# Kernel optimization log

Measured on AMD Instinct MI355X. Metric: run time of the kernel, lower is better.

## Reference

```python
import jax, jax.numpy as jnp
import numpy as np

B, N, F_IN, F_OUT, K, E = 4, 50000, 64, 64, 4, 800000


def setup_inputs() -> dict:
    key = jax.random.key(0)
    ks = jax.random.split(key, 6)
    x = jax.random.normal(ks[0], (B, N, F_IN), dtype=jnp.float32)
    support_rows = jax.random.randint(ks[1], (K, E), 0, N, dtype=jnp.int32)
    support_cols = jax.random.randint(ks[2], (K, E), 0, N, dtype=jnp.int32)
    support_vals = jax.random.normal(ks[3], (K, E), dtype=jnp.float32) * 0.1
    kernels = jax.random.normal(ks[4], (K, F_IN, F_OUT), dtype=jnp.float32) * (1.0 / np.sqrt(F_IN))
    bias = jnp.zeros((F_OUT,), dtype=jnp.float32)
    return {"x": x, "support_rows": support_rows, "support_cols": support_cols,
            "support_vals": support_vals, "kernels": kernels, "bias": bias}


def reference(x, support_rows, support_cols, support_vals, kernels, bias):
    # dropout_rate = 0.0 -> identity; sum_k support_k @ (x @ W_k) + bias, relu
    n = x.shape[1]
    out = jnp.zeros(x.shape[:2] + (kernels.shape[-1],), dtype=x.dtype)
    for k in range(kernels.shape[0]):  # small fixed K = 4 Chebyshev supports
        h = jnp.einsum('bnf,fg->bng', x, kernels[k])          # dense projection
        msg = h[:, support_cols[k], :] * support_vals[k][None, :, None]  # [B,E,G]
        agg = jax.ops.segment_sum(jnp.swapaxes(msg, 0, 1), support_rows[k],
                                  num_segments=n)              # [N,B,G]
        out = out + jnp.swapaxes(agg, 0, 1)
    return jax.nn.relu(out + bias)
```

## Files before the change

### kernel.cpp

```cpp
#include <hip/hip_runtime.h>


#define FDIM 64

__device__ __forceinline__ unsigned short bf16_rne(float v) {
    unsigned u = __float_as_uint(v);
    return (unsigned short)((u + 0x7FFFu + ((u >> 16) & 1u)) >> 16);
}

__global__ __launch_bounds__(256) void gemm_all(
    const float* __restrict__ x, const float* __restrict__ kernels,
    unsigned short* __restrict__ hb, int M, int kbase, int kcount)
{
    __shared__ float xs[64][68];
    __shared__ float Wl[64][64];

    const int t = threadIdx.x;
    const int row0 = blockIdx.x * 64;

#pragma unroll
    for (int i = 0; i < 4; ++i) {
        int idx = t + 256 * i;
        int r = idx >> 4;
        int c4 = idx & 15;
        float4 v = ((const float4*)(x + (size_t)(row0 + r) * FDIM))[c4];
        int f = c4 * 4;
        xs[f + 0][r] = v.x;
        xs[f + 1][r] = v.y;
        xs[f + 2][r] = v.z;
        xs[f + 3][r] = v.w;
    }

    const int r0 = (t >> 4) * 4;
    const int g0 = (t & 15) * 4;

    for (int kk = 0; kk < kcount; ++kk) {
        __syncthreads();
        {
            const float4* Wv = (const float4*)(kernels + (size_t)(kbase + kk) * FDIM * FDIM);
            float4* Wd = (float4*)&Wl[0][0];
#pragma unroll
            for (int i = 0; i < 4; ++i) Wd[t + 256 * i] = Wv[t + 256 * i];
        }
        __syncthreads();

        float acc[4][4];
#pragma unroll
        for (int i = 0; i < 4; ++i)
#pragma unroll
            for (int j = 0; j < 4; ++j) acc[i][j] = 0.f;

#pragma unroll
        for (int f = 0; f < 64; ++f) {
            float4 xv = *(const float4*)&xs[f][r0];
            float4 wv = *(const float4*)&Wl[f][g0];
            acc[0][0] = fmaf(xv.x, wv.x, acc[0][0]);
            acc[0][1] = fmaf(xv.x, wv.y, acc[0][1]);
            acc[0][2] = fmaf(xv.x, wv.z, acc[0][2]);
            acc[0][3] = fmaf(xv.x, wv.w, acc[0][3]);
            acc[1][0] = fmaf(xv.y, wv.x, acc[1][0]);
            acc[1][1] = fmaf(xv.y, wv.y, acc[1][1]);
            acc[1][2] = fmaf(xv.y, wv.z, acc[1][2]);
            acc[1][3] = fmaf(xv.y, wv.w, acc[1][3]);
            acc[2][0] = fmaf(xv.z, wv.x, acc[2][0]);
            acc[2][1] = fmaf(xv.z, wv.y, acc[2][1]);
            acc[2][2] = fmaf(xv.z, wv.z, acc[2][2]);
            acc[2][3] = fmaf(xv.z, wv.w, acc[2][3]);
            acc[3][0] = fmaf(xv.w, wv.x, acc[3][0]);
            acc[3][1] = fmaf(xv.w, wv.y, acc[3][1]);
            acc[3][2] = fmaf(xv.w, wv.z, acc[3][2]);
            acc[3][3] = fmaf(xv.w, wv.w, acc[3][3]);
        }

#pragma unroll
        for (int i = 0; i < 4; ++i) {
            ushort4 p;
            p.x = bf16_rne(acc[i][0]);
            p.y = bf16_rne(acc[i][1]);
            p.z = bf16_rne(acc[i][2]);
            p.w = bf16_rne(acc[i][3]);
            *(ushort4*)(hb + ((size_t)kk * M + row0 + r0 + i) * FDIM + g0) = p;
        }
    }
}

__global__ __launch_bounds__(256) void hist_rows(
    const int* __restrict__ rows, int* __restrict__ counts,
    int total, int E, int N)
{
    int i = blockIdx.x * 256 + threadIdx.x;
    if (i >= total) return;
    int k = i / E;
    atomicAdd(&counts[k * N + rows[i]], 1);
}

__global__ __launch_bounds__(256) void scan_block_sums(
    const int* __restrict__ counts, int* __restrict__ bsums, int N, int nb)
{
    int k = blockIdx.x / nb, j = blockIdx.x % nb;
    int t = threadIdx.x, lane = t & 63, w = t >> 6;
    int i = j * 256 + t;
    int v = (i < N) ? counts[k * N + i] : 0;
#pragma unroll
    for (int off = 32; off; off >>= 1) v += __shfl_down(v, off);
    __shared__ int lds[4];
    if (lane == 0) lds[w] = v;
    __syncthreads();
    if (t == 0) bsums[k * nb + j] = lds[0] + lds[1] + lds[2] + lds[3];
}

__global__ __launch_bounds__(256) void scan_bsums(int* bsums, int nb, int K)
{
    __shared__ int lds[4];
    __shared__ int carry;
    int t = threadIdx.x, lane = t & 63, w = t >> 6;
    for (int k = 0; k < K; ++k) {
        if (t == 0) carry = 0;
        __syncthreads();
        for (int base = 0; base < nb; base += 256) {
            int i = base + t;
            int v = (i < nb) ? bsums[k * nb + i] : 0;
            int x = v;
#pragma unroll
            for (int off = 1; off < 64; off <<= 1) {
                int y = __shfl_up(x, off);
                if (lane >= off) x += y;
            }
            if (lane == 63) lds[w] = x;
            __syncthreads();
            int wo = 0;
            for (int q = 0; q < w; ++q) wo += lds[q];
            int excl = carry + wo + x - v;
            if (i < nb) bsums[k * nb + i] = excl;
            __syncthreads();
            if (t == 255) carry = carry + wo + x;
            __syncthreads();
        }
    }
}

__global__ __launch_bounds__(256) void scan_write_ptr(
    const int* __restrict__ counts, const int* __restrict__ bsums,
    int* __restrict__ row_ptr, int N, int nb)
{
    int k = blockIdx.x / nb, j = blockIdx.x % nb;
    int t = threadIdx.x, lane = t & 63, w = t >> 6;
    int i = j * 256 + t;
    int v = (i < N) ? counts[k * N + i] : 0;
    int x = v;
#pragma unroll
    for (int off = 1; off < 64; off <<= 1) {
        int y = __shfl_up(x, off);
        if (lane >= off) x += y;
    }
    __shared__ int lds[4];
    if (lane == 63) lds[w] = x;
    __syncthreads();
    int wo = 0;
    for (int q = 0; q < w; ++q) wo += lds[q];
    int incl = wo + x;
    if (i < N) row_ptr[k * (N + 1) + i + 1] = bsums[k * nb + j] + incl;
    if (t == 0 && j == 0) row_ptr[k * (N + 1)] = 0;
}

__global__ __launch_bounds__(256) void fill_csr_packed(
    const int* __restrict__ rows, const int* __restrict__ cols,
    const float* __restrict__ vals, const int* __restrict__ row_ptr,
    int* __restrict__ counts, unsigned* __restrict__ csr,
    int total, int E, int N)
{
    int i = blockIdx.x * 256 + threadIdx.x;
    if (i >= total) return;
    int k = i / E;
    int row = rows[i];
    int old = atomicSub(&counts[k * N + row], 1);
    int slot = row_ptr[k * (N + 1) + row] + old - 1;
    unsigned pk = ((unsigned)cols[i] << 16) | (unsigned)bf16_rne(vals[i]);
    csr[(size_t)k * E + slot] = pk;
}

__global__ __launch_bounds__(256) void gather_fused(
    const unsigned short* __restrict__ hb, const int* __restrict__ row_ptr,
    const unsigned* __restrict__ csr, const float* __restrict__ bias,
    float* __restrict__ out, int N, int M, int E,
    int kbase, int kcount, int first, int last)
{
    const int wid = (blockIdx.x << 2) | (threadIdx.x >> 6);
    if (wid >= N) return;
    const int lane = threadIdx.x & 63;
    const int b = lane >> 4;
    const int c4 = lane & 15;

    float4 acc = make_float4(0.f, 0.f, 0.f, 0.f);

    for (int kk = 0; kk < kcount; ++kk) {
        const int* rp = row_ptr + (size_t)(kbase + kk) * (N + 1);
        const unsigned* ck = csr + (size_t)(kbase + kk) * E;
        const unsigned short* hbb =
            hb + ((size_t)kk * M + (size_t)b * N) * FDIM + c4 * 4;

        const int e0 = rp[wid];
        const int e1 = rp[wid + 1];

        for (int base = e0; base < e1; base += 64) {
            const int n = min(64, e1 - base);
            unsigned w = 0;
            if (lane < n) w = ck[base + lane];
            for (int j = 0; j < n; ++j) {
                unsigned ww = __shfl((int)w, j);
                int col = ww >> 16;
                float val = __uint_as_float(ww << 16);
                uint2 hv = *(const uint2*)(hbb + (size_t)col * FDIM);
                float f0 = __uint_as_float(hv.x << 16);
                float f1 = __uint_as_float(hv.x & 0xFFFF0000u);
                float f2 = __uint_as_float(hv.y << 16);
                float f3 = __uint_as_float(hv.y & 0xFFFF0000u);
                acc.x = fmaf(f0, val, acc.x);
                acc.y = fmaf(f1, val, acc.y);
                acc.z = fmaf(f2, val, acc.z);
                acc.w = fmaf(f3, val, acc.w);
            }
        }
    }

    float* op = out + ((size_t)b * N + wid) * FDIM + c4 * 4;
    if (first && last) {
        float4 bi = ((const float4*)bias)[c4];
        float4 o;
        o.x = fmaxf(acc.x + bi.x, 0.f);
        o.y = fmaxf(acc.y + bi.y, 0.f);
        o.z = fmaxf(acc.z + bi.z, 0.f);
        o.w = fmaxf(acc.w + bi.w, 0.f);
        *(float4*)op = o;
    } else if (first) {
        *(float4*)op = acc;
    } else if (!last) {
        float4 o = *(const float4*)op;
        o.x += acc.x; o.y += acc.y; o.z += acc.z; o.w += acc.w;
        *(float4*)op = o;
    } else {
        float4 o = *(const float4*)op;
        float4 bi = ((const float4*)bias)[c4];
        o.x = fmaxf(o.x + acc.x + bi.x, 0.f);
        o.y = fmaxf(o.y + acc.y + bi.y, 0.f);
        o.z = fmaxf(o.z + acc.z + bi.z, 0.f);
        o.w = fmaxf(o.w + acc.w + bi.w, 0.f);
        *(float4*)op = o;
    }
}

__global__ __launch_bounds__(256) void gemm64(
    const float* __restrict__ x, const float* __restrict__ W,
    float* __restrict__ h, int M)
{
    __shared__ float xs[64][68];
    __shared__ float Wl[64][64];
    const int t = threadIdx.x;
    {
        const float4* Wv = (const float4*)W;
        float4* Wd = (float4*)&Wl[0][0];
#pragma unroll
        for (int i = 0; i < 4; ++i) Wd[t + 256 * i] = Wv[t + 256 * i];
    }
    const int row0 = blockIdx.x * 64;
#pragma unroll
    for (int i = 0; i < 4; ++i) {
        int idx = t + 256 * i;
        int r = idx >> 4;
        int c4 = idx & 15;
        float4 v = ((const float4*)(x + (size_t)(row0 + r) * FDIM))[c4];
        int f = c4 * 4;
        xs[f + 0][r] = v.x; xs[f + 1][r] = v.y;
        xs[f + 2][r] = v.z; xs[f + 3][r] = v.w;
    }
    __syncthreads();
    const int r0 = (t >> 4) * 4;
    const int g0 = (t & 15) * 4;
    float acc[4][4];
#pragma unroll
    for (int i = 0; i < 4; ++i)
#pragma unroll
        for (int j = 0; j < 4; ++j) acc[i][j] = 0.f;
#pragma unroll
    for (int f = 0; f < 64; ++f) {
        float4 xv = *(const float4*)&xs[f][r0];
        float4 wv = *(const float4*)&Wl[f][g0];
        acc[0][0] = fmaf(xv.x, wv.x, acc[0][0]); acc[0][1] = fmaf(xv.x, wv.y, acc[0][1]);
        acc[0][2] = fmaf(xv.x, wv.z, acc[0][2]); acc[0][3] = fmaf(xv.x, wv.w, acc[0][3]);
        acc[1][0] = fmaf(xv.y, wv.x, acc[1][0]); acc[1][1] = fmaf(xv.y, wv.y, acc[1][1]);
        acc[1][2] = fmaf(xv.y, wv.z, acc[1][2]); acc[1][3] = fmaf(xv.y, wv.w, acc[1][3]);
        acc[2][0] = fmaf(xv.z, wv.x, acc[2][0]); acc[2][1] = fmaf(xv.z, wv.y, acc[2][1]);
        acc[2][2] = fmaf(xv.z, wv.z, acc[2][2]); acc[2][3] = fmaf(xv.z, wv.w, acc[2][3]);
        acc[3][0] = fmaf(xv.w, wv.x, acc[3][0]); acc[3][1] = fmaf(xv.w, wv.y, acc[3][1]);
        acc[3][2] = fmaf(xv.w, wv.z, acc[3][2]); acc[3][3] = fmaf(xv.w, wv.w, acc[3][3]);
    }
#pragma unroll
    for (int i = 0; i < 4; ++i)
        *(float4*)(h + (size_t)(row0 + r0 + i) * FDIM + g0) =
            make_float4(acc[i][0], acc[i][1], acc[i][2], acc[i][3]);
}

__global__ __launch_bounds__(256) void scatter_edges(
    const float* __restrict__ h, const int* __restrict__ rows,
    const int* __restrict__ cols, const float* __restrict__ vals,
    float* __restrict__ out, int E, int N)
{
    const int e = (blockIdx.x << 2) | (threadIdx.x >> 6);
    if (e >= E) return;
    const int lane = threadIdx.x & 63;
    const int row = __builtin_amdgcn_readfirstlane(rows[e]);
    const int col = __builtin_amdgcn_readfirstlane(cols[e]);
    const float val =
        __uint_as_float(__builtin_amdgcn_readfirstlane(__float_as_uint(vals[e])));
    const size_t stride = (size_t)N * FDIM;
    size_t cbase = (size_t)col * FDIM + lane;
    size_t rbase = (size_t)row * FDIM + lane;
#pragma unroll
    for (int b = 0; b < 4; ++b) {
        float hv = h[cbase + (size_t)b * stride];
        atomicAdd(out + rbase + (size_t)b * stride, hv * val);
    }
}

__global__ __launch_bounds__(256) void bias_relu(
    float* __restrict__ out, const float* __restrict__ bias, size_t total4)
{
    size_t i = (size_t)blockIdx.x * blockDim.x + threadIdx.x;
    if (i >= total4) return;
    float4 v = ((float4*)out)[i];
    float4 b = ((const float4*)bias)[i & 15];
    v.x = fmaxf(v.x + b.x, 0.f); v.y = fmaxf(v.y + b.y, 0.f);
    v.z = fmaxf(v.z + b.z, 0.f); v.w = fmaxf(v.w + b.w, 0.f);
    ((float4*)out)[i] = v;
}

extern "C" void kernel_launch(void* const* d_in, const int* in_sizes, int n_in,
                              void* d_out, int out_size, void* d_ws, size_t ws_size,
                              hipStream_t stream) {
    const float* x       = (const float*)d_in[0];
    const int*   rows    = (const int*)d_in[1];
    const int*   cols    = (const int*)d_in[2];
    const float* vals    = (const float*)d_in[3];
    const float* kernels = (const float*)d_in[4];
    const float* bias    = (const float*)d_in[5];

    float* out = (float*)d_out;

    const int K = in_sizes[4] / (FDIM * FDIM);
    const int E = in_sizes[1] / K;
    const int M = in_sizes[0] / FDIM;
    const int N = M / 4;
    const int total = K * E;
    const int nb = (N + 255) / 256;

    const size_t al = 15;
    const size_t csrB = ((size_t)total * 4 + al) & ~al;
    const size_t rpB  = ((size_t)K * (N + 1) * 4 + al) & ~al;
    const size_t cntB = ((size_t)K * N * 4 + al) & ~al;
    const size_t bsB  = ((size_t)K * nb * 4 + al) & ~al;
    const size_t baseB = csrB + rpB + cntB + bsB;
    const size_t planeB = (size_t)M * FDIM * 2;

    int G = 0;
    if (ws_size >= baseB + 4 * planeB) G = 4;
    else if (ws_size >= baseB + 2 * planeB) G = 2;
    else if (ws_size >= baseB + 1 * planeB) G = 1;

    if (G > 0) {
        char* ws = (char*)d_ws;
        unsigned short* hb = (unsigned short*)ws;  ws += (size_t)G * planeB;
        unsigned* csr      = (unsigned*)ws;        ws += csrB;
        int* row_ptr       = (int*)ws;             ws += rpB;
        int* counts        = (int*)ws;             ws += cntB;
        int* bsums         = (int*)ws;

        hipMemsetAsync(counts, 0, (size_t)K * N * 4, stream);
        hist_rows<<<(total + 255) / 256, 256, 0, stream>>>(rows, counts, total, E, N);
        scan_block_sums<<<K * nb, 256, 0, stream>>>(counts, bsums, N, nb);
        scan_bsums<<<1, 256, 0, stream>>>(bsums, nb, K);
        scan_write_ptr<<<K * nb, 256, 0, stream>>>(counts, bsums, row_ptr, N, nb);
        fill_csr_packed<<<(total + 255) / 256, 256, 0, stream>>>(
            rows, cols, vals, row_ptr, counts, csr, total, E, N);

        const int gblocks = (N + 3) / 4;
        for (int kb = 0; kb < K; kb += G) {
            const int kc = (kb + G <= K) ? G : (K - kb);
            gemm_all<<<M / 64, 256, 0, stream>>>(x, kernels, hb, M, kb, kc);
            gather_fused<<<gblocks, 256, 0, stream>>>(
                hb, row_ptr, csr, bias, out, N, M, E,
                kb, kc, kb == 0 ? 1 : 0, (kb + kc == K) ? 1 : 0);
        }
    } else {
        float* h = (float*)d_ws;
        hipMemsetAsync(out, 0, (size_t)out_size * sizeof(float), stream);
        for (int k = 0; k < K; ++k) {
            gemm64<<<M / 64, 256, 0, stream>>>(
                x, kernels + (size_t)k * FDIM * FDIM, h, M);
            scatter_edges<<<(E + 3) / 4, 256, 0, stream>>>(
                h, rows + (size_t)k * E, cols + (size_t)k * E,
                vals + (size_t)k * E, out, E, N);
        }
        const size_t total4 = (size_t)out_size / 4;
        bias_relu<<<(int)((total4 + 255) / 256), 256, 0, stream>>>(out, bias, total4);
    }
}
```

Baseline: 731.5 us.

## Reorder to aggregate-then-project with fused gather-GEMM and column-chunked CSR

Switches from projecting x by each W_k and then gathering, to gathering raw bf16 x rows (interleaved batch-major per node) for all four supports and then running one fused 256x64 GEMM per row with bias and ReLU. The CSR is also sorted by column chunk inside each row, which should make gather accesses more local. This removes the per-k GEMM passes, the intermediate h planes and the read-modify-write of the output. In exchange, x and W are rounded to bf16, the per-block LDS footprint is large (W plus accumulators), and there is a longer scan over K*N*CNUM segments.

```diff
diff --git a/kernel.cpp b/kernel.cpp
--- a/kernel.cpp
+++ b/kernel.cpp
@@ -2,96 +2,39 @@
 
 
 #define FDIM 64
+#define CHUNK_SHIFT 12
 
 __device__ __forceinline__ unsigned short bf16_rne(float v) {
     unsigned u = __float_as_uint(v);
     return (unsigned short)((u + 0x7FFFu + ((u >> 16) & 1u)) >> 16);
 }
 
-__global__ __launch_bounds__(256) void gemm_all(
-    const float* __restrict__ x, const float* __restrict__ kernels,
-    unsigned short* __restrict__ hb, int M, int kbase, int kcount)
-{
-    __shared__ float xs[64][68];
-    __shared__ float Wl[64][64];
-
-    const int t = threadIdx.x;
-    const int row0 = blockIdx.x * 64;
-
-#pragma unroll
-    for (int i = 0; i < 4; ++i) {
-        int idx = t + 256 * i;
-        int r = idx >> 4;
-        int c4 = idx & 15;
-        float4 v = ((const float4*)(x + (size_t)(row0 + r) * FDIM))[c4];
-        int f = c4 * 4;
-        xs[f + 0][r] = v.x;
-        xs[f + 1][r] = v.y;
-        xs[f + 2][r] = v.z;
-        xs[f + 3][r] = v.w;
-    }
-
-    const int r0 = (t >> 4) * 4;
-    const int g0 = (t & 15) * 4;
-
-    for (int kk = 0; kk < kcount; ++kk) {
-        __syncthreads();
-        {
-            const float4* Wv = (const float4*)(kernels + (size_t)(kbase + kk) * FDIM * FDIM);
-            float4* Wd = (float4*)&Wl[0][0];
-#pragma unroll
-            for (int i = 0; i < 4; ++i) Wd[t + 256 * i] = Wv[t + 256 * i];
-        }
-        __syncthreads();
-
-        float acc[4][4];
-#pragma unroll
-        for (int i = 0; i < 4; ++i)
-#pragma unroll
-            for (int j = 0; j < 4; ++j) acc[i][j] = 0.f;
-
-#pragma unroll
-        for (int f = 0; f < 64; ++f) {
-            float4 xv = *(const float4*)&xs[f][r0];
-            float4 wv = *(const float4*)&Wl[f][g0];
-            acc[0][0] = fmaf(xv.x, wv.x, acc[0][0]);
-            acc[0][1] = fmaf(xv.x, wv.y, acc[0][1]);
-            acc[0][2] = fmaf(xv.x, wv.z, acc[0][2]);
-            acc[0][3] = fmaf(xv.x, wv.w, acc[0][3]);
-            acc[1][0] = fmaf(xv.y, wv.x, acc[1][0]);
-            acc[1][1] = fmaf(xv.y, wv.y, acc[1][1]);
-            acc[1][2] = fmaf(xv.y, wv.z, acc[1][2]);
-            acc[1][3] = fmaf(xv.y, wv.w, acc[1][3]);
-            acc[2][0] = fmaf(xv.z, wv.x, acc[2][0]);
-            acc[2][1] = fmaf(xv.z, wv.y, acc[2][1]);
-            acc[2][2] = fmaf(xv.z, wv.z, acc[2][2]);
-            acc[2][3] = fmaf(xv.z, wv.w, acc[2][3]);
-            acc[3][0] = fmaf(xv.w, wv.x, acc[3][0]);
-            acc[3][1] = fmaf(xv.w, wv.y, acc[3][1]);
-            acc[3][2] = fmaf(xv.w, wv.z, acc[3][2]);
-            acc[3][3] = fmaf(xv.w, wv.w, acc[3][3]);
-        }
-
-#pragma unroll
-        for (int i = 0; i < 4; ++i) {
-            ushort4 p;
-            p.x = bf16_rne(acc[i][0]);
-            p.y = bf16_rne(acc[i][1]);
-            p.z = bf16_rne(acc[i][2]);
-            p.w = bf16_rne(acc[i][3]);
-            *(ushort4*)(hb + ((size_t)kk * M + row0 + r0 + i) * FDIM + g0) = p;
-        }
-    }
-}
-
-__global__ __launch_bounds__(256) void hist_rows(
-    const int* __restrict__ rows, int* __restrict__ counts,
-    int total, int E, int N)
+__global__ __launch_bounds__(256) void pack_x(
+    const float* __restrict__ x, unsigned short* __restrict__ xb,
+    int M, int N)
+{
+    int i = blockIdx.x * 256 + threadIdx.x;
+    if (i >= M * 16) return;
+    int f4 = i & 15;
+    int bn = i >> 4;
+    int b = bn / N;
+    int n = bn - b * N;
+    float4 v = ((const float4*)x)[i];
+    ushort4 p;
+    p.x = bf16_rne(v.x); p.y = bf16_rne(v.y);
+    p.z = bf16_rne(v.z); p.w = bf16_rne(v.w);
+    *(ushort4*)(xb + (size_t)n * 256 + b * 64 + f4 * 4) = p;
+}
+
+__global__ __launch_bounds__(256) void hist2(
+    const int* __restrict__ rows, const int* __restrict__ cols,
+    int* __restrict__ counts2, int total, int E, int N, int CNUM)
 {
     int i = blockIdx.x * 256 + threadIdx.x;
     if (i >= total) return;
     int k = i / E;
-    atomicAdd(&counts[k * N + rows[i]], 1);
+    int idx = (k * N + rows[i]) * CNUM + (cols[i] >> CHUNK_SHIFT);
+    atomicAdd(&counts2[idx], 1);
 }
 
 __global__ __launch_bounds__(256) void scan_block_sums(
@@ -141,7 +84,7 @@
 
 __global__ __launch_bounds__(256) void scan_write_ptr(
     const int* __restrict__ counts, const int* __restrict__ bsums,
-    int* __restrict__ row_ptr, int N, int nb)
+    int* __restrict__ ptr, int N, int nb)
 {
     int k = blockIdx.x / nb, j = blockIdx.x % nb;
     int t = threadIdx.x, lane = t & 63, w = t >> 6;
@@ -159,93 +102,106 @@
     int wo = 0;
     for (int q = 0; q < w; ++q) wo += lds[q];
     int incl = wo + x;
-    if (i < N) row_ptr[k * (N + 1) + i + 1] = bsums[k * nb + j] + incl;
-    if (t == 0 && j == 0) row_ptr[k * (N + 1)] = 0;
-}
-
-__global__ __launch_bounds__(256) void fill_csr_packed(
+    if (i < N) ptr[k * (N + 1) + i + 1] = bsums[k * nb + j] + incl;
+    if (t == 0 && j == 0) ptr[k * (N + 1)] = 0;
+}
+
+__global__ __launch_bounds__(256) void fill2(
     const int* __restrict__ rows, const int* __restrict__ cols,
-    const float* __restrict__ vals, const int* __restrict__ row_ptr,
-    int* __restrict__ counts, unsigned* __restrict__ csr,
-    int total, int E, int N)
+    const float* __restrict__ vals, const int* __restrict__ seg_ptr,
+    int* __restrict__ counts2, unsigned* __restrict__ csr,
+    int total, int E, int N, int CNUM)
 {
     int i = blockIdx.x * 256 + threadIdx.x;
     if (i >= total) return;
     int k = i / E;
-    int row = rows[i];
-    int old = atomicSub(&counts[k * N + row], 1);
-    int slot = row_ptr[k * (N + 1) + row] + old - 1;
-    unsigned pk = ((unsigned)cols[i] << 16) | (unsigned)bf16_rne(vals[i]);
-    csr[(size_t)k * E + slot] = pk;
-}
-
-__global__ __launch_bounds__(256) void gather_fused(
-    const unsigned short* __restrict__ hb, const int* __restrict__ row_ptr,
-    const unsigned* __restrict__ csr, const float* __restrict__ bias,
-    float* __restrict__ out, int N, int M, int E,
-    int kbase, int kcount, int first, int last)
-{
-    const int wid = (blockIdx.x << 2) | (threadIdx.x >> 6);
-    if (wid >= N) return;
-    const int lane = threadIdx.x & 63;
+    int col = cols[i];
+    int idx = (k * N + rows[i]) * CNUM + (col >> CHUNK_SHIFT);
+    int old = atomicSub(&counts2[idx], 1);
+    int slot = seg_ptr[idx] + old - 1;
+    csr[slot] = ((unsigned)col << 16) | (unsigned)bf16_rne(vals[i]);
+}
+
+__global__ __launch_bounds__(256) void gather_gemm(
+    const unsigned short* __restrict__ xb,
+    const int* __restrict__ seg_ptr,
+    const unsigned* __restrict__ csr,
+    const float* __restrict__ kernels,
+    const float* __restrict__ bias,
+    float* __restrict__ out,
+    int N, int CNUM)
+{
+    __shared__ unsigned short Wl[256 * 64];
+    __shared__ float accS[4][4][260];
+
+    const int t = threadIdx.x;
+
+#pragma unroll
+    for (int i = 0; i < 16; ++i) {
+        int idx = t + 256 * i;
+        float4 v = ((const float4*)kernels)[idx];
+        ushort4 p;
+        p.x = bf16_rne(v.x); p.y = bf16_rne(v.y);
+        p.z = bf16_rne(v.z); p.w = bf16_rne(v.w);
+        ((ushort4*)Wl)[idx] = p;
+    }
+    __syncthreads();
+
+    const int w = t >> 6, lane = t & 63;
+    const int row = blockIdx.x * 4 + w;
     const int b = lane >> 4;
-    const int c4 = lane & 15;
-
-    float4 acc = make_float4(0.f, 0.f, 0.f, 0.f);
-
-    for (int kk = 0; kk < kcount; ++kk) {
-        const int* rp = row_ptr + (size_t)(kbase + kk) * (N + 1);
-        const unsigned* ck = csr + (size_t)(kbase + kk) * E;
-        const unsigned short* hbb =
-            hb + ((size_t)kk * M + (size_t)b * N) * FDIM + c4 * 4;
-
-        const int e0 = rp[wid];
-        const int e1 = rp[wid + 1];
-
-        for (int base = e0; base < e1; base += 64) {
-            const int n = min(64, e1 - base);
-            unsigned w = 0;
-            if (lane < n) w = ck[base + lane];
-            for (int j = 0; j < n; ++j) {
-                unsigned ww = __shfl((int)w, j);
+    const int q4 = lane & 15;
+
+    if (row < N) {
+        const unsigned short* xbl = xb + lane * 4;
+        float4 acc[4];
+#pragma unroll
+        for (int k = 0; k < 4; ++k) acc[k] = make_float4(0.f, 0.f, 0.f, 0.f);
+
+#pragma unroll
+        for (int k = 0; k < 4; ++k) {
+            const int e0 = seg_ptr[(k * N + row) * CNUM];
+            const int e1 = seg_ptr[(k * N + row + 1) * CNUM];
+#pragma unroll 8
+            for (int j = e0; j < e1; ++j) {
+                unsigned ww = csr[j];
                 int col = ww >> 16;
                 float val = __uint_as_float(ww << 16);
-                uint2 hv = *(const uint2*)(hbb + (size_t)col * FDIM);
+                uint2 hv = *(const uint2*)(xbl + (size_t)col * 256);
                 float f0 = __uint_as_float(hv.x << 16);
                 float f1 = __uint_as_float(hv.x & 0xFFFF0000u);
                 float f2 = __uint_as_float(hv.y << 16);
                 float f3 = __uint_as_float(hv.y & 0xFFFF0000u);
-                acc.x = fmaf(f0, val, acc.x);
-                acc.y = fmaf(f1, val, acc.y);
-                acc.z = fmaf(f2, val, acc.z);
-                acc.w = fmaf(f3, val, acc.w);
+                acc[k].x = fmaf(f0, val, acc[k].x);
+                acc[k].y = fmaf(f1, val, acc[k].y);
+                acc[k].z = fmaf(f2, val, acc[k].z);
+                acc[k].w = fmaf(f3, val, acc[k].w);
             }
         }
-    }
-
-    float* op = out + ((size_t)b * N + wid) * FDIM + c4 * 4;
-    if (first && last) {
-        float4 bi = ((const float4*)bias)[c4];
-        float4 o;
-        o.x = fmaxf(acc.x + bi.x, 0.f);
-        o.y = fmaxf(acc.y + bi.y, 0.f);
-        o.z = fmaxf(acc.z + bi.z, 0.f);
-        o.w = fmaxf(acc.w + bi.w, 0.f);
-        *(float4*)op = o;
-    } else if (first) {
-        *(float4*)op = acc;
-    } else if (!last) {
-        float4 o = *(const float4*)op;
-        o.x += acc.x; o.y += acc.y; o.z += acc.z; o.w += acc.w;
-        *(float4*)op = o;
-    } else {
-        float4 o = *(const float4*)op;
-        float4 bi = ((const float4*)bias)[c4];
-        o.x = fmaxf(o.x + acc.x + bi.x, 0.f);
-        o.y = fmaxf(o.y + acc.y + bi.y, 0.f);
-        o.z = fmaxf(o.z + acc.z + bi.z, 0.f);
-        o.w = fmaxf(o.w + acc.w + bi.w, 0.f);
-        *(float4*)op = o;
+
+#pragma unroll
+        for (int k = 0; k < 4; ++k)
+            *(float4*)&accS[w][b][k * 64 + q4 * 4] = acc[k];
+    }
+    __syncthreads();
+
+    if (row < N) {
+        float4 o = make_float4(0.f, 0.f, 0.f, 0.f);
+#pragma unroll 4
+        for (int kf = 0; kf < 256; ++kf) {
+            float a = accS[w][b][kf];
+            ushort4 wv = *(const ushort4*)&Wl[kf * 64 + q4 * 4];
+            o.x = fmaf(a, __uint_as_float((unsigned)wv.x << 16), o.x);
+            o.y = fmaf(a, __uint_as_float((unsigned)wv.y << 16), o.y);
+            o.z = fmaf(a, __uint_as_float((unsigned)wv.z << 16), o.z);
+            o.w = fmaf(a, __uint_as_float((unsigned)wv.w << 16), o.w);
+        }
+        float4 bi = ((const float4*)bias)[q4];
+        o.x = fmaxf(o.x + bi.x, 0.f);
+        o.y = fmaxf(o.y + bi.y, 0.f);
+        o.z = fmaxf(o.z + bi.z, 0.f);
+        o.w = fmaxf(o.w + bi.w, 0.f);
+        *(float4*)(out + ((size_t)b * N + row) * 64 + q4 * 4) = o;
     }
 }
 
@@ -351,45 +307,43 @@
     const int M = in_sizes[0] / FDIM;
     const int N = M / 4;
     const int total = K * E;
-    const int nb = (N + 255) / 256;
+
+    const int CNUM = (N + (1 << CHUNK_SHIFT) - 1) >> CHUNK_SHIFT;
+    const long long L = (long long)K * N * CNUM;
+    const int nb2 = (int)((L + 255) / 256);
 
     const size_t al = 15;
-    const size_t csrB = ((size_t)total * 4 + al) & ~al;
-    const size_t rpB  = ((size_t)K * (N + 1) * 4 + al) & ~al;
-    const size_t cntB = ((size_t)K * N * 4 + al) & ~al;
-    const size_t bsB  = ((size_t)K * nb * 4 + al) & ~al;
-    const size_t baseB = csrB + rpB + cntB + bsB;
-    const size_t planeB = (size_t)M * FDIM * 2;
-
-    int G = 0;
-    if (ws_size >= baseB + 4 * planeB) G = 4;
-    else if (ws_size >= baseB + 2 * planeB) G = 2;
-    else if (ws_size >= baseB + 1 * planeB) G = 1;
-
-    if (G > 0) {
+    const size_t xbB  = (((size_t)N * 512) + al) & ~al;
+    const size_t csrB = (((size_t)total * 4) + al) & ~al;
+    const size_t segB = (((size_t)(L + 1) * 4) + al) & ~al;
+    const size_t cntB = (((size_t)L * 4) + al) & ~al;
+    const size_t bsB  = (((size_t)nb2 * 4) + al) & ~al;
+    const size_t needed = xbB + csrB + segB + cntB + bsB;
+
+    const bool fast = (K == 4) && (N <= 65536) && (M == 4 * N) &&
+                      (ws_size >= needed) && (L < (1LL << 31));
+
+    if (fast) {
         char* ws = (char*)d_ws;
-        unsigned short* hb = (unsigned short*)ws;  ws += (size_t)G * planeB;
-        unsigned* csr      = (unsigned*)ws;        ws += csrB;
-        int* row_ptr       = (int*)ws;             ws += rpB;
-        int* counts        = (int*)ws;             ws += cntB;
-        int* bsums         = (int*)ws;
-
-        hipMemsetAsync(counts, 0, (size_t)K * N * 4, stream);
-        hist_rows<<<(total + 255) / 256, 256, 0, stream>>>(rows, counts, total, E, N);
-        scan_block_sums<<<K * nb, 256, 0, stream>>>(counts, bsums, N, nb);
-        scan_bsums<<<1, 256, 0, stream>>>(bsums, nb, K);
-        scan_write_ptr<<<K * nb, 256, 0, stream>>>(counts, bsums, row_ptr, N, nb);
-        fill_csr_packed<<<(total + 255) / 256, 256, 0, stream>>>(
-            rows, cols, vals, row_ptr, counts, csr, total, E, N);
-
-        const int gblocks = (N + 3) / 4;
-        for (int kb = 0; kb < K; kb += G) {
-            const int kc = (kb + G <= K) ? G : (K - kb);
-            gemm_all<<<M / 64, 256, 0, stream>>>(x, kernels, hb, M, kb, kc);
-            gather_fused<<<gblocks, 256, 0, stream>>>(
-                hb, row_ptr, csr, bias, out, N, M, E,
-                kb, kc, kb == 0 ? 1 : 0, (kb + kc == K) ? 1 : 0);
-        }
+        unsigned short* xb  = (unsigned short*)ws;  ws += xbB;
+        unsigned* csr       = (unsigned*)ws;        ws += csrB;
+        int* seg_ptr        = (int*)ws;             ws += segB;
+        int* counts2        = (int*)ws;             ws += cntB;
+        int* bsums2         = (int*)ws;
+
+        pack_x<<<(M * 16 + 255) / 256, 256, 0, stream>>>(x, xb, M, N);
+
+        hipMemsetAsync(counts2, 0, (size_t)L * 4, stream);
+        hist2<<<(total + 255) / 256, 256, 0, stream>>>(
+            rows, cols, counts2, total, E, N, CNUM);
+        scan_block_sums<<<nb2, 256, 0, stream>>>(counts2, bsums2, (int)L, nb2);
+        scan_bsums<<<1, 256, 0, stream>>>(bsums2, nb2, 1);
+        scan_write_ptr<<<nb2, 256, 0, stream>>>(counts2, bsums2, seg_ptr, (int)L, nb2);
+        fill2<<<(total + 255) / 256, 256, 0, stream>>>(
+            rows, cols, vals, seg_ptr, counts2, csr, total, E, N, CNUM);
+
+        gather_gemm<<<(N + 3) / 4, 256, 0, stream>>>(
+            xb, seg_ptr, csr, kernels, bias, out, N, CNUM);
     } else {
         float* h = (float*)d_ws;
         hipMemsetAsync(out, 0, (size_t)out_size * sizeof(float), stream);
```

Result: slower. 882.4 us (+20.6%).
